# Optimization experiments

Hardware: AMD Instinct MI355X
Metric: run time of the kernel (lower is better)

The kernel has to match this reference:

```python
import jax, jax.numpy as jnp
import numpy as np

B, S, D, H = 1, 4096, 1024, 16
HD = D // H  # head_dim = 64
NEG = -1e9

def setup_inputs() -> dict:
    key = jax.random.key(0)
    ks = jax.random.split(key, 5)
    scale = 1.0 / np.sqrt(D)
    x = jax.random.normal(ks[0], (B, S, D), dtype=jnp.float32)
    Wq = jax.random.normal(ks[1], (D, D), dtype=jnp.float32) * scale
    Wk = jax.random.normal(ks[2], (D, D), dtype=jnp.float32) * scale
    Wv = jax.random.normal(ks[3], (D, D), dtype=jnp.float32) * scale
    Wo = jax.random.normal(ks[4], (D, D), dtype=jnp.float32) * scale
    mask = jnp.tril(jnp.ones((S, S), dtype=bool))[None, None]  # [1,1,S,S] causal
    return {"x": x, "mask": mask, "Wq": Wq, "Wk": Wk, "Wv": Wv, "Wo": Wo}

def reference(x, mask, Wq, Wk, Wv, Wo):
    # Linear projections (bias=False). nn.Linear computes x @ W.T; weights here
    # are stored as [out, in] so we use x @ W.T for faithfulness.
    q = x @ Wq.T  # [B,S,D]
    k = x @ Wk.T
    v = x @ Wv.T
    def split_heads(t):
        return t.reshape(B, S, H, HD).transpose(0, 2, 1, 3)  # [B,H,S,HD]
    q, k, v = split_heads(q), split_heads(k), split_heads(v)
    scores = jnp.einsum("bhqd,bhkd->bhqk", q, k) / jnp.sqrt(jnp.float32(HD))
    scores = jnp.where(mask, scores, NEG)
    attn = jax.nn.softmax(scores, axis=-1)  # dropout p=0.0 -> identity
    out = jnp.einsum("bhqk,bhkd->bhqd", attn, v)  # [B,H,S,HD]
    out = out.transpose(0, 2, 1, 3).reshape(B, S, D)
    return out @ Wo.T
```

## Files before the change

### kernel.cpp

```cpp
#include <hip/hip_runtime.h>
#include <hip/hip_bf16.h>


typedef __bf16 bf16x8 __attribute__((ext_vector_type(8)));
typedef __bf16 bf16x4 __attribute__((ext_vector_type(4)));
typedef float f32x4 __attribute__((ext_vector_type(4)));
typedef short s16x4 __attribute__((ext_vector_type(4)));

#define GAS __attribute__((address_space(1)))
#define LAS __attribute__((address_space(3)))

__device__ __forceinline__ void async_copy16(const void* g, void* l) {
  __builtin_amdgcn_global_load_lds((const GAS unsigned int*)g,
                                   (LAS unsigned int*)l, 16, 0, 0);
}

__device__ __forceinline__ f32x4 mfma_k16(bf16x4 a, bf16x4 b, f32x4 c) {
  union { bf16x4 h; s16x4 s; } ua, ub;
  ua.h = a; ub.h = b;
  return __builtin_amdgcn_mfma_f32_16x16x16bf16_1k(ua.s, ub.s, c, 0, 0, 0);
}

__global__ __launch_bounds__(256) void cvt_all(const float* __restrict__ x,
                                               const float* __restrict__ Wq,
                                               const float* __restrict__ Wk,
                                               const float* __restrict__ Wv,
                                               const float* __restrict__ Wo,
                                               __bf16* __restrict__ xb,
                                               __bf16* __restrict__ Wc,
                                               __bf16* __restrict__ Wob) {
  int b = blockIdx.x;
  const float* src;
  __bf16* dst;
  if (b < 4096)      { src = x  + (b       ) * 1024; dst = xb  + (long)b * 1024; }
  else if (b < 5120) { src = Wq + (b - 4096) * 1024; dst = Wc  + (long)(b - 4096) * 1024; }
  else if (b < 6144) { src = Wk + (b - 5120) * 1024; dst = Wc  + (1l << 20) + (long)(b - 5120) * 1024; }
  else if (b < 7168) { src = Wv + (b - 6144) * 1024; dst = Wc  + (2l << 20) + (long)(b - 6144) * 1024; }
  else               { src = Wo + (b - 7168) * 1024; dst = Wob + (long)(b - 7168) * 1024; }
  int i = threadIdx.x * 4;
  float4 f = *(const float4*)(src + i);
  bf16x4 o;
  o[0] = (__bf16)f.x; o[1] = (__bf16)f.y; o[2] = (__bf16)f.z; o[3] = (__bf16)f.w;
  *(bf16x4*)(dst + i) = o;
}

__global__ __launch_bounds__(256) void gemm_qkv(const __bf16* __restrict__ A,
                                                const __bf16* __restrict__ B,
                                                __bf16* __restrict__ Qb,
                                                __bf16* __restrict__ Kf,
                                                __bf16* __restrict__ Vf) {
  const int K = 1024;
  __shared__ __bf16 As[128 * 32];
  __shared__ __bf16 Bs[128 * 32];
  const int tid = threadIdx.x;
  const int lane = tid & 63, wv = tid >> 6;
  const int l15 = lane & 15, quad = lane >> 4;
  const int wm = wv >> 1, wn = wv & 1;
  const int mbase = blockIdx.y * 128, nbase = blockIdx.x * 128;
  const bool kswap = (nbase >= 1024) && (nbase < 2048);

  f32x4 acc[4][4] = {};

  for (int k0 = 0; k0 < K; k0 += 32) {
    __syncthreads();
#pragma unroll
    for (int q = 0; q < 2; ++q) {
      int i = q * 256 + tid;
      int row = i >> 2, kg = i & 3;
      const __bf16* ga = A + (long)(mbase + row) * K + k0 + kg * 8;
      const __bf16* gb = B + (long)(nbase + row) * K + k0 + kg * 8;
      char* la = (char*)As + (q * 256 + wv * 64) * 16;
      char* lb = (char*)Bs + (q * 256 + wv * 64) * 16;
      async_copy16(ga, la);
      async_copy16(gb, lb);
    }
    __syncthreads();
    bf16x8 af[4], bfr[4];
#pragma unroll
    for (int i = 0; i < 4; ++i)
      af[i] = *(const bf16x8*)&As[(wm * 64 + i * 16 + l15) * 32 + quad * 8];
#pragma unroll
    for (int j = 0; j < 4; ++j)
      bfr[j] = *(const bf16x8*)&Bs[(wn * 64 + j * 16 + l15) * 32 + quad * 8];
    if (kswap) {
#pragma unroll
      for (int i = 0; i < 4; ++i)
#pragma unroll
        for (int j = 0; j < 4; ++j)
          acc[i][j] = __builtin_amdgcn_mfma_f32_16x16x32_bf16(bfr[j], af[i], acc[i][j], 0, 0, 0);
    } else {
#pragma unroll
      for (int i = 0; i < 4; ++i)
#pragma unroll
        for (int j = 0; j < 4; ++j)
          acc[i][j] = __builtin_amdgcn_mfma_f32_16x16x32_bf16(af[i], bfr[j], acc[i][j], 0, 0, 0);
    }
  }

  if (nbase < 1024) {
    const float QS = 0.18033688011112043f;
#pragma unroll
    for (int i = 0; i < 4; ++i)
#pragma unroll
      for (int j = 0; j < 4; ++j) {
        int col = nbase + wn * 64 + j * 16 + l15;
#pragma unroll
        for (int r = 0; r < 4; ++r) {
          int row = mbase + wm * 64 + i * 16 + quad * 4 + r;
          Qb[(long)row * 1024 + col] = (__bf16)(acc[i][j][r] * QS);
        }
      }
  } else if (nbase < 2048) {
#pragma unroll
    for (int i = 0; i < 4; ++i)
#pragma unroll
      for (int j = 0; j < 4; ++j) {
        int d0 = nbase - 1024 + wn * 64 + j * 16 + quad * 4;
        int h = d0 >> 6, dd = d0 & 63;
        int kk = dd >> 5, qf = (dd >> 3) & 3, e0 = dd & 7;
        int kt = mbase + wm * 64 + i * 16 + l15;
        int tile = kt >> 6;
        long off = ((long)(h * 64 + tile) * 8 + i * 2 + kk) * 512 + (qf * 16 + l15) * 8 + e0;
        union { __bf16 b[4]; uint2 u; } pk;
#pragma unroll
        for (int r = 0; r < 4; ++r) pk.b[r] = (__bf16)acc[i][j][r];
        *(uint2*)(Kf + off) = pk.u;
      }
  } else {
#pragma unroll
    for (int i = 0; i < 4; ++i)
#pragma unroll
      for (int j = 0; j < 4; ++j) {
        int col = nbase - 2048 + wn * 64 + j * 16 + l15;
        int h = col >> 6, dd = col & 63;
        int jd = dd >> 4, lv = dd & 15;
        int kt0 = mbase + wm * 64 + i * 16 + quad * 4;
        int tile = kt0 >> 6, w6 = kt0 & 63;
        int jp = w6 >> 5, bit4 = (w6 >> 4) & 1, qv = (w6 >> 2) & 3;
        long off = ((long)(h * 64 + tile) * 8 + jd * 2 + jp) * 512 + (qv * 16 + lv) * 8 + bit4 * 4;
        union { __bf16 b[4]; uint2 u; } pk;
#pragma unroll
        for (int r = 0; r < 4; ++r) pk.b[r] = (__bf16)acc[i][j][r];
        *(uint2*)(Vf + off) = pk.u;
      }
  }
}

__global__ __launch_bounds__(256) void gemm_wo(const __bf16* __restrict__ A,
                                               const __bf16* __restrict__ B,
                                               float* __restrict__ C) {
  const int K = 1024, N = 1024;
  __shared__ __bf16 As[128 * 32];
  __shared__ __bf16 Bs[64 * 32];
  const int tid = threadIdx.x;
  const int lane = tid & 63, wv = tid >> 6;
  const int l15 = lane & 15, quad = lane >> 4;
  const int wm = wv >> 1, wn = wv & 1;
  const int mbase = blockIdx.y * 128, nbase = blockIdx.x * 64;

  f32x4 acc[4][2] = {};

  for (int k0 = 0; k0 < K; k0 += 32) {
    __syncthreads();
#pragma unroll
    for (int q = 0; q < 2; ++q) {
      int i = q * 256 + tid;
      int row = i >> 2, kg = i & 3;
      const __bf16* ga = A + (long)(mbase + row) * K + k0 + kg * 8;
      char* la = (char*)As + (q * 256 + wv * 64) * 16;
      async_copy16(ga, la);
    }
    {
      int row = tid >> 2, kg = tid & 3;
      const __bf16* gb = B + (long)(nbase + row) * K + k0 + kg * 8;
      char* lb = (char*)Bs + (wv * 64) * 16;
      async_copy16(gb, lb);
    }
    __syncthreads();
    bf16x8 af[4], bfr[2];
#pragma unroll
    for (int i = 0; i < 4; ++i)
      af[i] = *(const bf16x8*)&As[(wm * 64 + i * 16 + l15) * 32 + quad * 8];
#pragma unroll
    for (int j = 0; j < 2; ++j)
      bfr[j] = *(const bf16x8*)&Bs[(wn * 32 + j * 16 + l15) * 32 + quad * 8];
#pragma unroll
    for (int i = 0; i < 4; ++i)
#pragma unroll
      for (int j = 0; j < 2; ++j)
        acc[i][j] = __builtin_amdgcn_mfma_f32_16x16x32_bf16(af[i], bfr[j], acc[i][j], 0, 0, 0);
  }
#pragma unroll
  for (int i = 0; i < 4; ++i)
#pragma unroll
    for (int j = 0; j < 2; ++j)
#pragma unroll
      for (int r = 0; r < 4; ++r) {
        int row = mbase + wm * 64 + i * 16 + quad * 4 + r;
        int col = nbase + wn * 32 + j * 16 + l15;
        C[(long)row * N + col] = acc[i][j][r];
      }
}

__global__ __launch_bounds__(512, 2) void flash_attn(const __bf16* __restrict__ Qb,
                                                     const __bf16* __restrict__ Kf,
                                                     const __bf16* __restrict__ Vf,
                                                     __bf16* __restrict__ AO) {
  __shared__ float Ms[2][3][64][34];
  const int tid = threadIdx.x;
  const int lane = tid & 63, l15 = lane & 15, quad = lane >> 4;
  const int w = tid >> 6;
  const int pr = w >> 2, qtr = w & 3;
  const int b = blockIdx.x;
  const int h = (b & 7) + 8 * ((b >> 3) & 1);
  const int rest = b >> 4;
  const int P = rest * 2 + pr;
  const int hoff = h * 64;

  const __bf16* Kh = Kf + (long)h * 64 * 4096;
  const __bf16* Vh = Vf + (long)h * 64 * 4096;

  for (int pass = 0; pass < 2; ++pass) {
    const int T = pass ? (127 - P) : P;
    bf16x8 qf[2][2];
#pragma unroll
    for (int g = 0; g < 2; ++g) {
      const int qrow = T * 32 + g * 16 + l15;
      qf[g][0] = *(const bf16x8*)(Qb + (long)qrow * 1024 + hoff + quad * 8);
      qf[g][1] = *(const bf16x8*)(Qb + (long)qrow * 1024 + hoff + 32 + quad * 8);
    }

    const int nkt = (T >> 1) + 1;
    const int kt0 = (nkt * qtr) >> 2;
    const int kt1 = (nkt * (qtr + 1)) >> 2;
    f32x4 o_acc[2][4] = {};
    float l_acc[2] = {0.0f, 0.0f};

    bf16x8 kc[8];
    if (kt0 < kt1) {
      const __bf16* Kt = Kh + (long)kt0 * 4096;
#pragma unroll
      for (int f = 0; f < 8; ++f)
        kc[f] = *(const bf16x8*)(Kt + f * 512 + lane * 8);
    }

    for (int kt = kt0; kt < kt1; ++kt) {
      const __bf16* Vt = Vh + (long)kt * 4096;

      bf16x8 va[8];
#pragma unroll
      for (int f = 0; f < 8; ++f)
        va[f] = *(const bf16x8*)(Vt + f * 512 + lane * 8);

      f32x4 st[2][4] = {};
#pragma unroll
      for (int g = 0; g < 2; ++g)
#pragma unroll
        for (int j = 0; j < 4; ++j) {
          st[g][j] = __builtin_amdgcn_mfma_f32_16x16x32_bf16(kc[j * 2 + 0], qf[g][0], st[g][j], 0, 0, 0);
          st[g][j] = __builtin_amdgcn_mfma_f32_16x16x32_bf16(kc[j * 2 + 1], qf[g][1], st[g][j], 0, 0, 0);
        }

      if (kt + 1 < kt1) {
        const __bf16* Kt = Kh + (long)(kt + 1) * 4096;
#pragma unroll
        for (int f = 0; f < 8; ++f)
          kc[f] = *(const bf16x8*)(Kt + f * 512 + lane * 8);
      }

      if (kt == nkt - 1) {
#pragma unroll
        for (int g = 0; g < 2; ++g) {
          const int dq = (T & 1) * 32 + g * 16 + l15;
#pragma unroll
          for (int j = 0; j < 4; ++j)
#pragma unroll
            for (int r = 0; r < 4; ++r)
              if (j * 16 + quad * 4 + r > dq) st[g][j][r] = -3.0e38f;
        }
      }

      bf16x4 pb[2][4];
#pragma unroll
      for (int g = 0; g < 2; ++g) {
        float ps = 0.0f;
#pragma unroll
        for (int j = 0; j < 4; ++j) {
          f32x4 pj;
#pragma unroll
          for (int r = 0; r < 4; ++r) pj[r] = __builtin_amdgcn_exp2f(st[g][j][r]);
          ps += (pj[0] + pj[1]) + (pj[2] + pj[3]);
          bf16x4 bb;
#pragma unroll
          for (int r = 0; r < 4; ++r) bb[r] = (__bf16)pj[r];
          pb[g][j] = bb;
        }
        l_acc[g] += ps;
      }

#pragma unroll
      for (int g = 0; g < 2; ++g)
#pragma unroll
        for (int j = 0; j < 4; ++j) {
          bf16x4 pbj = pb[g][j];
#pragma unroll
          for (int jd = 0; jd < 4; ++jd) {
            bf16x8 v8 = va[jd * 2 + (j >> 1)];
            bf16x4 a4 = (j & 1) ? __builtin_shufflevector(v8, v8, 4, 5, 6, 7)
                                : __builtin_shufflevector(v8, v8, 0, 1, 2, 3);
            o_acc[g][jd] = mfma_k16(a4, pbj, o_acc[g][jd]);
          }
        }
    }

    if (qtr) {
#pragma unroll
      for (int g = 0; g < 2; ++g) {
#pragma unroll
        for (int jd = 0; jd < 4; ++jd)
#pragma unroll
          for (int r = 0; r < 4; ++r)
            Ms[pr][qtr - 1][lane][g * 16 + jd * 4 + r] = o_acc[g][jd][r];
        Ms[pr][qtr - 1][lane][32 + g] = l_acc[g];
      }
    }
    __syncthreads();
    if (!qtr) {
#pragma unroll
      for (int g = 0; g < 2; ++g) {
        float la = l_acc[g];
#pragma unroll
        for (int s = 0; s < 3; ++s) {
#pragma unroll
          for (int jd = 0; jd < 4; ++jd)
#pragma unroll
            for (int r = 0; r < 4; ++r)
              o_acc[g][jd][r] += Ms[pr][s][lane][g * 16 + jd * 4 + r];
          la += Ms[pr][s][lane][32 + g];
        }
        la += __shfl_xor(la, 16);
        la += __shfl_xor(la, 32);
        const float inv = 1.0f / la;
        const int qrow = T * 32 + g * 16 + l15;
#pragma unroll
        for (int jd = 0; jd < 4; ++jd) {
          bf16x4 ob;
#pragma unroll
          for (int r = 0; r < 4; ++r) ob[r] = (__bf16)(o_acc[g][jd][r] * inv);
          *(bf16x4*)(AO + (long)qrow * 1024 + hoff + jd * 16 + quad * 4) = ob;
        }
      }
    }
    __syncthreads();
  }
}

extern "C" void kernel_launch(void* const* d_in, const int* in_sizes, int n_in,
                              void* d_out, int out_size, void* d_ws, size_t ws_size,
                              hipStream_t stream) {
  const float* x  = (const float*)d_in[0];
  const float* Wq = (const float*)d_in[2];
  const float* Wk = (const float*)d_in[3];
  const float* Wv = (const float*)d_in[4];
  const float* Wo = (const float*)d_in[5];
  float* out = (float*)d_out;

  char* ws = (char*)d_ws;
  __bf16* xb  = (__bf16*)ws;
  __bf16* Wc  = (__bf16*)(ws + (8u << 20));
  __bf16* Wob = (__bf16*)(ws + (14u << 20));
  __bf16* Qb  = (__bf16*)(ws + (16u << 20));
  __bf16* Kfr = (__bf16*)(ws + (24u << 20));
  __bf16* Vfr = (__bf16*)(ws + (32u << 20));
  __bf16* AO  = (__bf16*)(ws + (40u << 20));

  cvt_all<<<8192, 256, 0, stream>>>(x, Wq, Wk, Wv, Wo, xb, Wc, Wob);

  dim3 g1(3072 / 128, 4096 / 128);
  gemm_qkv<<<g1, 256, 0, stream>>>(xb, Wc, Qb, Kfr, Vfr);

  flash_attn<<<512, 512, 0, stream>>>(Qb, Kfr, Vfr, AO);

  dim3 g2(1024 / 64, 4096 / 128);
  gemm_wo<<<g2, 256, 0, stream>>>(AO, Wob, out);
}
```

Baseline: 238.9 us.

## Widen flash attention query tile to 64 rows per wave for K/V reuse

Each wave now handles 64 query rows instead of 32, so every loaded K/V tile feeds twice as many MFMAs and total K/V global traffic is halved. The grid shrinks from 512 to 256 blocks. Score computation and exp/convert are interleaved per 16-row group to limit register pressure. The cross-wave reduction uses a smaller shared buffer written with vector stores and serialised over the two wave sets, which adds extra barriers. Fewer blocks and higher register use may lower occupancy and worsen load balance on the causal triangle.

```diff
diff --git a/kernel.cpp b/kernel.cpp
--- a/kernel.cpp
+++ b/kernel.cpp
@@ -206,35 +206,35 @@
                                                      const __bf16* __restrict__ Kf,
                                                      const __bf16* __restrict__ Vf,
                                                      __bf16* __restrict__ AO) {
-  __shared__ float Ms[2][3][64][34];
+  __shared__ float Ms[3][64][76];
   const int tid = threadIdx.x;
   const int lane = tid & 63, l15 = lane & 15, quad = lane >> 4;
   const int w = tid >> 6;
-  const int pr = w >> 2, qtr = w & 3;
+  const int s = w >> 2, qtr = w & 3;
   const int b = blockIdx.x;
   const int h = (b & 7) + 8 * ((b >> 3) & 1);
   const int rest = b >> 4;
-  const int P = rest * 2 + pr;
+  const int P = rest * 2 + s;
   const int hoff = h * 64;
 
   const __bf16* Kh = Kf + (long)h * 64 * 4096;
   const __bf16* Vh = Vf + (long)h * 64 * 4096;
 
   for (int pass = 0; pass < 2; ++pass) {
-    const int T = pass ? (127 - P) : P;
-    bf16x8 qf[2][2];
-#pragma unroll
-    for (int g = 0; g < 2; ++g) {
-      const int qrow = T * 32 + g * 16 + l15;
+    const int T = pass ? (63 - P) : P;
+    bf16x8 qf[4][2];
+#pragma unroll
+    for (int g = 0; g < 4; ++g) {
+      const int qrow = T * 64 + g * 16 + l15;
       qf[g][0] = *(const bf16x8*)(Qb + (long)qrow * 1024 + hoff + quad * 8);
       qf[g][1] = *(const bf16x8*)(Qb + (long)qrow * 1024 + hoff + 32 + quad * 8);
     }
 
-    const int nkt = (T >> 1) + 1;
+    const int nkt = T + 1;
     const int kt0 = (nkt * qtr) >> 2;
     const int kt1 = (nkt * (qtr + 1)) >> 2;
-    f32x4 o_acc[2][4] = {};
-    float l_acc[2] = {0.0f, 0.0f};
+    f32x4 o_acc[4][4] = {};
+    float l_acc[4] = {0.0f, 0.0f, 0.0f, 0.0f};
 
     bf16x8 kc[8];
     if (kt0 < kt1) {
@@ -252,14 +252,39 @@
       for (int f = 0; f < 8; ++f)
         va[f] = *(const bf16x8*)(Vt + f * 512 + lane * 8);
 
-      f32x4 st[2][4] = {};
-#pragma unroll
-      for (int g = 0; g < 2; ++g)
+      bf16x4 pb[4][4];
+#pragma unroll
+      for (int g = 0; g < 4; ++g) {
+        f32x4 stg[4] = {};
 #pragma unroll
         for (int j = 0; j < 4; ++j) {
-          st[g][j] = __builtin_amdgcn_mfma_f32_16x16x32_bf16(kc[j * 2 + 0], qf[g][0], st[g][j], 0, 0, 0);
-          st[g][j] = __builtin_amdgcn_mfma_f32_16x16x32_bf16(kc[j * 2 + 1], qf[g][1], st[g][j], 0, 0, 0);
-        }
+          stg[j] = __builtin_amdgcn_mfma_f32_16x16x32_bf16(kc[j * 2 + 0], qf[g][0], stg[j], 0, 0, 0);
+          stg[j] = __builtin_amdgcn_mfma_f32_16x16x32_bf16(kc[j * 2 + 1], qf[g][1], stg[j], 0, 0, 0);
+        }
+
+        if (kt == nkt - 1) {
+          const int dq = g * 16 + l15;
+#pragma unroll
+          for (int j = 0; j < 4; ++j)
+#pragma unroll
+            for (int r = 0; r < 4; ++r)
+              if (j * 16 + quad * 4 + r > dq) stg[j][r] = -3.0e38f;
+        }
+
+        float ps = 0.0f;
+#pragma unroll
+        for (int j = 0; j < 4; ++j) {
+          f32x4 pj;
+#pragma unroll
+          for (int r = 0; r < 4; ++r) pj[r] = __builtin_amdgcn_exp2f(stg[j][r]);
+          ps += (pj[0] + pj[1]) + (pj[2] + pj[3]);
+          bf16x4 bb;
+#pragma unroll
+          for (int r = 0; r < 4; ++r) bb[r] = (__bf16)pj[r];
+          pb[g][j] = bb;
+        }
+        l_acc[g] += ps;
+      }
 
       if (kt + 1 < kt1) {
         const __bf16* Kt = Kh + (long)(kt + 1) * 4096;
@@ -268,38 +293,8 @@
           kc[f] = *(const bf16x8*)(Kt + f * 512 + lane * 8);
       }
 
-      if (kt == nkt - 1) {
-#pragma unroll
-        for (int g = 0; g < 2; ++g) {
-          const int dq = (T & 1) * 32 + g * 16 + l15;
-#pragma unroll
-          for (int j = 0; j < 4; ++j)
-#pragma unroll
-            for (int r = 0; r < 4; ++r)
-              if (j * 16 + quad * 4 + r > dq) st[g][j][r] = -3.0e38f;
-        }
-      }
-
-      bf16x4 pb[2][4];
-#pragma unroll
-      for (int g = 0; g < 2; ++g) {
-        float ps = 0.0f;
-#pragma unroll
-        for (int j = 0; j < 4; ++j) {
-          f32x4 pj;
-#pragma unroll
-          for (int r = 0; r < 4; ++r) pj[r] = __builtin_amdgcn_exp2f(st[g][j][r]);
-          ps += (pj[0] + pj[1]) + (pj[2] + pj[3]);
-          bf16x4 bb;
-#pragma unroll
-          for (int r = 0; r < 4; ++r) bb[r] = (__bf16)pj[r];
-          pb[g][j] = bb;
-        }
-        l_acc[g] += ps;
-      }
-
-#pragma unroll
-      for (int g = 0; g < 2; ++g)
+#pragma unroll
+      for (int g = 0; g < 4; ++g)
 #pragma unroll
         for (int j = 0; j < 4; ++j) {
           bf16x4 pbj = pb[g][j];
@@ -313,45 +308,45 @@
         }
     }
 
-    if (qtr) {
-#pragma unroll
-      for (int g = 0; g < 2; ++g) {
-#pragma unroll
-        for (int jd = 0; jd < 4; ++jd)
-#pragma unroll
-          for (int r = 0; r < 4; ++r)
-            Ms[pr][qtr - 1][lane][g * 16 + jd * 4 + r] = o_acc[g][jd][r];
-        Ms[pr][qtr - 1][lane][32 + g] = l_acc[g];
-      }
-    }
-    __syncthreads();
-    if (!qtr) {
-#pragma unroll
-      for (int g = 0; g < 2; ++g) {
-        float la = l_acc[g];
-#pragma unroll
-        for (int s = 0; s < 3; ++s) {
+    for (int ms = 0; ms < 2; ++ms) {
+      if (s == ms && qtr) {
+#pragma unroll
+        for (int g = 0; g < 4; ++g)
 #pragma unroll
           for (int jd = 0; jd < 4; ++jd)
-#pragma unroll
-            for (int r = 0; r < 4; ++r)
-              o_acc[g][jd][r] += Ms[pr][s][lane][g * 16 + jd * 4 + r];
-          la += Ms[pr][s][lane][32 + g];
-        }
-        la += __shfl_xor(la, 16);
-        la += __shfl_xor(la, 32);
-        const float inv = 1.0f / la;
-        const int qrow = T * 32 + g * 16 + l15;
-#pragma unroll
-        for (int jd = 0; jd < 4; ++jd) {
-          bf16x4 ob;
-#pragma unroll
-          for (int r = 0; r < 4; ++r) ob[r] = (__bf16)(o_acc[g][jd][r] * inv);
-          *(bf16x4*)(AO + (long)qrow * 1024 + hoff + jd * 16 + quad * 4) = ob;
-        }
-      }
-    }
-    __syncthreads();
+            *(f32x4*)&Ms[qtr - 1][lane][g * 16 + jd * 4] = o_acc[g][jd];
+        f32x4 lv;
+#pragma unroll
+        for (int g = 0; g < 4; ++g) lv[g] = l_acc[g];
+        *(f32x4*)&Ms[qtr - 1][lane][64] = lv;
+      }
+      __syncthreads();
+      if (s == ms && !qtr) {
+#pragma unroll
+        for (int g = 0; g < 4; ++g) {
+          float la = l_acc[g];
+#pragma unroll
+          for (int u = 0; u < 3; ++u) {
+#pragma unroll
+            for (int jd = 0; jd < 4; ++jd)
+              o_acc[g][jd] += *(const f32x4*)&Ms[u][lane][g * 16 + jd * 4];
+            la += Ms[u][lane][64 + g];
+          }
+          la += __shfl_xor(la, 16);
+          la += __shfl_xor(la, 32);
+          const float inv = 1.0f / la;
+          const int qrow = T * 64 + g * 16 + l15;
+#pragma unroll
+          for (int jd = 0; jd < 4; ++jd) {
+            bf16x4 ob;
+#pragma unroll
+            for (int r = 0; r < 4; ++r) ob[r] = (__bf16)(o_acc[g][jd][r] * inv);
+            *(bf16x4*)(AO + (long)qrow * 1024 + hoff + jd * 16 + quad * 4) = ob;
+          }
+        }
+      }
+      __syncthreads();
+    }
   }
 }
 
@@ -379,7 +374,7 @@
   dim3 g1(3072 / 128, 4096 / 128);
   gemm_qkv<<<g1, 256, 0, stream>>>(xb, Wc, Qb, Kfr, Vfr);
 
-  flash_attn<<<512, 512, 0, stream>>>(Qb, Kfr, Vfr, AO);
+  flash_attn<<<256, 512, 0, stream>>>(Qb, Kfr, Vfr, AO);
 
   dim3 g2(1024 / 64, 4096 / 128);
   gemm_wo<<<g2, 256, 0, stream>>>(AO, Wob, out);
```

After: 238.0 us. No clear change (-0.4%).
